# Optimization experiments

Measured on AMD Instinct MI355X. Metric: run time of the kernel, lower is better.

Reference implementation:

```python
import jax, jax.numpy as jnp
import numpy as np

ALPHA = 0.2  # LeakyReLU negative slope
NEG_BIG = -9e15


def setup_inputs() -> dict:
    key = jax.random.key(0)
    k1, k2, k3, k4 = jax.random.split(key, 4)
    N, F_IN, F_OUT = 8192, 256, 64
    h = jax.random.normal(k1, (N, F_IN), dtype=jnp.float32)
    # binary dense adjacency (density ~0.5), kept as float32 as in the torch code
    adj = jax.random.randint(k2, (N, N), 0, 2).astype(jnp.float32)
    W = jax.random.normal(k3, (F_IN, F_OUT), dtype=jnp.float32) * 0.05
    a = jax.random.normal(k4, (2 * F_OUT, 1), dtype=jnp.float32) * 0.05
    return {"h": h, "adj": adj, "W": W, "a": a}


def reference(h, adj, W, a):
    F_OUT = W.shape[1]
    Wh = h @ W                               # [N, F]
    # Decomposed concat-attention score: e_ij = LeakyReLU(a1.Wh_i + a2.Wh_j)
    f_src = Wh @ a[:F_OUT, 0]                # [N]
    f_dst = Wh @ a[F_OUT:, 0]                # [N]
    e = f_src[:, None] + f_dst[None, :]      # [N, N]
    e = jnp.where(e > 0, e, ALPHA * e)       # LeakyReLU
    e = jnp.where(adj > 0, e, NEG_BIG)       # mask non-edges
    attention = jax.nn.softmax(e, axis=1)    # row softmax (dropout p=0 -> identity)
    h_prime = attention @ (adj @ Wh)         # note: double propagation as in source
    # concat=True -> ELU
    return jnp.where(h_prime > 0, h_prime, jnp.expm1(h_prime))
```

## Files before the change

kernel.cpp:

```cpp
#include <hip/hip_runtime.h>
#include <hip/hip_bf16.h>


#define N 8192

typedef float f32x4 __attribute__((ext_vector_type(4)));
typedef short s16x8 __attribute__((ext_vector_type(8)));
typedef unsigned long long u64;
typedef u64 u64x2 __attribute__((ext_vector_type(2)));

__device__ __forceinline__ unsigned short f2bf(float x) {
  unsigned u = __float_as_uint(x);
  u += 0x7FFFu + ((u >> 16) & 1u);
  return (unsigned short)(u >> 16);
}
__device__ __forceinline__ unsigned pack2(unsigned short lo, unsigned short hi) {
  return (unsigned)lo | ((unsigned)hi << 16);
}

#define MFMA __builtin_amdgcn_mfma_f32_16x16x32_bf16

__global__ __launch_bounds__(256) void kA(const float* __restrict__ adj,
                                          const float* __restrict__ h,
                                          const float* __restrict__ W,
                                          const float* __restrict__ a,
                                          u64* __restrict__ ML,
                                          unsigned short* __restrict__ Bpack,
                                          float* __restrict__ f,
                                          float* __restrict__ g,
                                          float* __restrict__ expg,
                                          float* __restrict__ expg2) {
  const int l = threadIdx.x & 63;
  const int w = threadIdx.x >> 6;
  const int i = (blockIdx.x << 1) + (w & 1);
  if (w < 2) {
    const float* ap = adj + (size_t)i * N + (l << 2);
    u64* mp = ML + (size_t)i * 128;
    f32x4 v0 = *(const f32x4*)(ap);
    f32x4 v1 = *(const f32x4*)(ap + 256);
    f32x4 v2 = *(const f32x4*)(ap + 512);
    f32x4 v3 = *(const f32x4*)(ap + 768);
    for (int cc = 0; cc < 32; cc += 4) {
      const int cn = (cc < 28) ? (cc + 4) : cc;
      f32x4 n0 = *(const f32x4*)(ap + ((cn + 0) << 8));
      f32x4 n1 = *(const f32x4*)(ap + ((cn + 1) << 8));
      f32x4 n2 = *(const f32x4*)(ap + ((cn + 2) << 8));
      f32x4 n3 = *(const f32x4*)(ap + ((cn + 3) << 8));
      u64 b0  = __ballot(v0.x > 0.f), b1  = __ballot(v0.y > 0.f);
      u64 b2  = __ballot(v0.z > 0.f), b3  = __ballot(v0.w > 0.f);
      u64 b4  = __ballot(v1.x > 0.f), b5  = __ballot(v1.y > 0.f);
      u64 b6  = __ballot(v1.z > 0.f), b7  = __ballot(v1.w > 0.f);
      u64 b8  = __ballot(v2.x > 0.f), b9  = __ballot(v2.y > 0.f);
      u64 b10 = __ballot(v2.z > 0.f), b11 = __ballot(v2.w > 0.f);
      u64 b12 = __ballot(v3.x > 0.f), b13 = __ballot(v3.y > 0.f);
      u64 b14 = __ballot(v3.z > 0.f), b15 = __ballot(v3.w > 0.f);
      if (l == 0) {
        u64x2* q = (u64x2*)(mp + (cc << 2));
        u64x2 t0; t0.x = b0;  t0.y = b1;  q[0] = t0;
        u64x2 t1; t1.x = b2;  t1.y = b3;  q[1] = t1;
        u64x2 t2; t2.x = b4;  t2.y = b5;  q[2] = t2;
        u64x2 t3; t3.x = b6;  t3.y = b7;  q[3] = t3;
        u64x2 t4; t4.x = b8;  t4.y = b9;  q[4] = t4;
        u64x2 t5; t5.x = b10; t5.y = b11; q[5] = t5;
        u64x2 t6; t6.x = b12; t6.y = b13; q[6] = t6;
        u64x2 t7; t7.x = b14; t7.y = b15; q[7] = t7;
      }
      v0 = n0; v1 = n1; v2 = n2; v3 = n3;
    }
  } else {
    const float* hrow = h + (size_t)i * 256;
    float acc = 0.f;
#pragma unroll 4
    for (int kb = 0; kb < 64; ++kb) {
      f32x4 hv = *(const f32x4*)(hrow + (kb << 2));
      acc += hv.x * W[((kb << 2) + 0) * 64 + l];
      acc += hv.y * W[((kb << 2) + 1) * 64 + l];
      acc += hv.z * W[((kb << 2) + 2) * 64 + l];
      acc += hv.w * W[((kb << 2) + 3) * 64 + l];
    }
    float s1 = acc * a[l];
    float s2 = acc * a[64 + l];
#pragma unroll
    for (int d = 32; d > 0; d >>= 1) {
      s1 += __shfl_xor(s1, d);
      s2 += __shfl_xor(s2, d);
    }
    if (l == 0) {
      f[i] = s1; g[i] = s2;
      expg[i] = __expf(s2);
      expg2[i] = __expf(0.2f * s2);
    }
    const int kb = i >> 5;
    const int b = l >> 4;
    const int lp = (l & 15) | (((i >> 3) & 3) << 4);
    const int e = i & 7;
    Bpack[(((size_t)(kb * 4 + b)) * 64 + lp) * 8 + e] = f2bf(acc);
  }
}

__global__ __launch_bounds__(512) void k2b(const u64* __restrict__ ML,
                                           const unsigned short* __restrict__ Bpack,
                                           const float* __restrict__ g,
                                           const float* __restrict__ f,
                                           unsigned short* __restrict__ Upack,
                                           float* __restrict__ Av,
                                           float* __restrict__ Cv) {
  __shared__ float red[2][8][64][16];
  __shared__ float gred[2][8][16];
  const int l = threadIdx.x & 63;
  const int w = threadIdx.x >> 6;
  const int i0 = blockIdx.x << 5;
  const int r = l & 15, kg = l >> 4;
  const s16x8* Bv = (const s16x8*)Bpack;
  const u64x2* mrow0 = (const u64x2*)(ML + (size_t)(i0 + r) * 128);
  const u64x2* mrow1 = (const u64x2*)(ML + (size_t)(i0 + 16 + r) * 128);
  const int sh0 = kg << 1;
  f32x4 x0 = {0.f,0.f,0.f,0.f}, x1 = x0, x2 = x0, x3 = x0;
  f32x4 y0 = x0, y1 = x0, y2 = x0, y3 = x0;
  float gmx0 = -INFINITY, gmx1 = -INFINITY;
  for (int cc = 0; cc < 4; ++cc) {
    const int c = (w << 2) + cc;
    u64x2 ma = mrow0[(c << 1)], mb = mrow0[(c << 1) + 1];
    const u64 xa0 = ma.x >> sh0, xa1 = ma.y >> sh0,
              xa2 = mb.x >> sh0, xa3 = mb.y >> sh0;
    u64x2 mc = mrow1[(c << 1)], md = mrow1[(c << 1) + 1];
    const u64 ya0 = mc.x >> sh0, ya1 = mc.y >> sh0,
              ya2 = md.x >> sh0, ya3 = md.y >> sh0;
#pragma unroll
    for (int j7 = 0; j7 < 8; ++j7) {
      const int jb = (c << 3) + j7;
      f32x4 g0 = *(const f32x4*)(g + (jb << 5) + (kg << 3));
      f32x4 g1 = *(const f32x4*)(g + (jb << 5) + (kg << 3) + 4);
      const unsigned p0 = (unsigned)(xa0 >> (j7 << 3)) & 1u;
      const unsigned p1 = (unsigned)(xa1 >> (j7 << 3)) & 1u;
      const unsigned p2 = (unsigned)(xa2 >> (j7 << 3)) & 1u;
      const unsigned p3 = (unsigned)(xa3 >> (j7 << 3)) & 1u;
      const unsigned p4 = (unsigned)(xa0 >> ((j7 << 3) + 1)) & 1u;
      const unsigned p5 = (unsigned)(xa1 >> ((j7 << 3) + 1)) & 1u;
      const unsigned p6 = (unsigned)(xa2 >> ((j7 << 3) + 1)) & 1u;
      const unsigned p7 = (unsigned)(xa3 >> ((j7 << 3) + 1)) & 1u;
      const unsigned q0 = (unsigned)(ya0 >> (j7 << 3)) & 1u;
      const unsigned q1 = (unsigned)(ya1 >> (j7 << 3)) & 1u;
      const unsigned q2 = (unsigned)(ya2 >> (j7 << 3)) & 1u;
      const unsigned q3 = (unsigned)(ya3 >> (j7 << 3)) & 1u;
      const unsigned q4 = (unsigned)(ya0 >> ((j7 << 3) + 1)) & 1u;
      const unsigned q5 = (unsigned)(ya1 >> ((j7 << 3) + 1)) & 1u;
      const unsigned q6 = (unsigned)(ya2 >> ((j7 << 3) + 1)) & 1u;
      const unsigned q7 = (unsigned)(ya3 >> ((j7 << 3) + 1)) & 1u;
      s16x8 af0, af1;
      af0[0] = p0 ? (short)0x3F80 : (short)0;
      af0[1] = p1 ? (short)0x3F80 : (short)0;
      af0[2] = p2 ? (short)0x3F80 : (short)0;
      af0[3] = p3 ? (short)0x3F80 : (short)0;
      af0[4] = p4 ? (short)0x3F80 : (short)0;
      af0[5] = p5 ? (short)0x3F80 : (short)0;
      af0[6] = p6 ? (short)0x3F80 : (short)0;
      af0[7] = p7 ? (short)0x3F80 : (short)0;
      af1[0] = q0 ? (short)0x3F80 : (short)0;
      af1[1] = q1 ? (short)0x3F80 : (short)0;
      af1[2] = q2 ? (short)0x3F80 : (short)0;
      af1[3] = q3 ? (short)0x3F80 : (short)0;
      af1[4] = q4 ? (short)0x3F80 : (short)0;
      af1[5] = q5 ? (short)0x3F80 : (short)0;
      af1[6] = q6 ? (short)0x3F80 : (short)0;
      af1[7] = q7 ? (short)0x3F80 : (short)0;
      if (p0) gmx0 = fmaxf(gmx0, g0.x);
      if (p1) gmx0 = fmaxf(gmx0, g0.y);
      if (p2) gmx0 = fmaxf(gmx0, g0.z);
      if (p3) gmx0 = fmaxf(gmx0, g0.w);
      if (p4) gmx0 = fmaxf(gmx0, g1.x);
      if (p5) gmx0 = fmaxf(gmx0, g1.y);
      if (p6) gmx0 = fmaxf(gmx0, g1.z);
      if (p7) gmx0 = fmaxf(gmx0, g1.w);
      if (q0) gmx1 = fmaxf(gmx1, g0.x);
      if (q1) gmx1 = fmaxf(gmx1, g0.y);
      if (q2) gmx1 = fmaxf(gmx1, g0.z);
      if (q3) gmx1 = fmaxf(gmx1, g0.w);
      if (q4) gmx1 = fmaxf(gmx1, g1.x);
      if (q5) gmx1 = fmaxf(gmx1, g1.y);
      if (q6) gmx1 = fmaxf(gmx1, g1.z);
      if (q7) gmx1 = fmaxf(gmx1, g1.w);
      const size_t bi = ((size_t)jb << 8) + l;
      s16x8 f0 = Bv[bi], f1 = Bv[bi + 64], f2 = Bv[bi + 128], f3 = Bv[bi + 192];
      x0 = MFMA(af0, f0, x0, 0, 0, 0);
      x1 = MFMA(af0, f1, x1, 0, 0, 0);
      x2 = MFMA(af0, f2, x2, 0, 0, 0);
      x3 = MFMA(af0, f3, x3, 0, 0, 0);
      y0 = MFMA(af1, f0, y0, 0, 0, 0);
      y1 = MFMA(af1, f1, y1, 0, 0, 0);
      y2 = MFMA(af1, f2, y2, 0, 0, 0);
      y3 = MFMA(af1, f3, y3, 0, 0, 0);
    }
  }
  gmx0 = fmaxf(gmx0, __shfl_xor(gmx0, 16));
  gmx0 = fmaxf(gmx0, __shfl_xor(gmx0, 32));
  gmx1 = fmaxf(gmx1, __shfl_xor(gmx1, 16));
  gmx1 = fmaxf(gmx1, __shfl_xor(gmx1, 32));
  if (l < 16) { gred[0][w][l] = gmx0; gred[1][w][l] = gmx1; }
#pragma unroll
  for (int q = 0; q < 4; ++q) {
    red[0][w][l][q] = x0[q]; red[0][w][l][4 + q] = x1[q];
    red[0][w][l][8 + q] = x2[q]; red[0][w][l][12 + q] = x3[q];
    red[1][w][l][q] = y0[q]; red[1][w][l][4 + q] = y1[q];
    red[1][w][l][8 + q] = y2[q]; red[1][w][l][12 + q] = y3[q];
  }
  __syncthreads();
  const int tl = threadIdx.x & 63;
  const int b = (threadIdx.x >> 6) & 3;
  const int sE = threadIdx.x >> 8;
  const int reg0 = sE << 1;
#pragma unroll
  for (int s = 0; s < 2; ++s) {
    float u0 = 0.f, u1 = 0.f;
#pragma unroll
    for (int w8 = 0; w8 < 8; ++w8) {
      u0 += red[s][w8][tl][(b << 2) + reg0];
      u1 += red[s][w8][tl][(b << 2) + reg0 + 1];
    }
    const int k0 = i0 + (s << 4) + ((tl >> 4) << 2) + reg0;
    const unsigned pkv = pack2(f2bf(u0), f2bf(u1));
    const int kbD = k0 >> 5, lgrp = (k0 >> 3) & 3, e0 = k0 & 7;
    *(unsigned*)((char*)Upack +
        ((size_t)((kbD << 2) + b) * 64 + ((tl & 15) | (lgrp << 4))) * 16 + (e0 << 1)) = pkv;
  }
  if (threadIdx.x < 32) {
    const int s2 = threadIdx.x >> 4, rr = threadIdx.x & 15;
    float gm = gred[s2][0][rr];
#pragma unroll
    for (int w8 = 1; w8 < 8; ++w8) gm = fmaxf(gm, gred[s2][w8][rr]);
    const int i = i0 + (s2 << 4) + rr;
    const float fv = f[i];
    float mm = fv + gm;
    mm = fmaxf(mm, 0.2f * mm);
    Av[i] = __expf(fv - mm);
    Cv[i] = __expf(0.2f * fv - mm);
  }
}

__global__ __launch_bounds__(512) void k3(const u64* __restrict__ ML,
                                          const unsigned short* __restrict__ Upack,
                                          const float* __restrict__ f,
                                          const float* __restrict__ expg,
                                          const float* __restrict__ expg2,
                                          const float* __restrict__ Av,
                                          const float* __restrict__ Cv,
                                          float* __restrict__ out) {
  __shared__ float red[2][8][64][16];
  __shared__ float wred[2][8][16];
  const int l = threadIdx.x & 63;
  const int w = threadIdx.x >> 6;
  const int i0 = blockIdx.x << 5;
  const int r = l & 15, kg = l >> 4;
  const float enf0 = __expf(-f[i0 + r]);
  const float enf1 = __expf(-f[i0 + 16 + r]);
  const float Ar0 = Av[i0 + r],      Cr0 = Cv[i0 + r];
  const float Ar1 = Av[i0 + 16 + r], Cr1 = Cv[i0 + 16 + r];
  const s16x8* Uv = (const s16x8*)Upack;
  const u64x2* mrow0 = (const u64x2*)(ML + (size_t)(i0 + r) * 128);
  const u64x2* mrow1 = (const u64x2*)(ML + (size_t)(i0 + 16 + r) * 128);
  const int sh0 = kg << 1;
  f32x4 x0 = {0.f,0.f,0.f,0.f}, x1 = x0, x2 = x0, x3 = x0;
  f32x4 y0 = x0, y1 = x0, y2 = x0, y3 = x0;
  float ws0 = 0.f, ws1 = 0.f;
  for (int cc = 0; cc < 4; ++cc) {
    const int c = (w << 2) + cc;
    u64x2 ma = mrow0[(c << 1)], mb = mrow0[(c << 1) + 1];
    const u64 xa0 = ma.x >> sh0, xa1 = ma.y >> sh0,
              xa2 = mb.x >> sh0, xa3 = mb.y >> sh0;
    u64x2 mc = mrow1[(c << 1)], md = mrow1[(c << 1) + 1];
    const u64 ya0 = mc.x >> sh0, ya1 = mc.y >> sh0,
              ya2 = md.x >> sh0, ya3 = md.y >> sh0;
#pragma unroll
    for (int j7 = 0; j7 < 8; ++j7) {
      const int jb = (c << 3) + j7;
      f32x4 eg0 = *(const f32x4*)(expg + (jb << 5) + (kg << 3));
      f32x4 eg1 = *(const f32x4*)(expg + (jb << 5) + (kg << 3) + 4);
      f32x4 eh0 = *(const f32x4*)(expg2 + (jb << 5) + (kg << 3));
      f32x4 eh1 = *(const f32x4*)(expg2 + (jb << 5) + (kg << 3) + 4);
      s16x8 pf0, pf1;
#define K3W(pf, idx, wq, sh, egv, ehv, enf, Ar, Cr, wsv) {   \
      const unsigned bit_ = (unsigned)((wq) >> (sh)) & 1u;   \
      const bool sg_ = (egv) > (enf);                        \
      float t_ = sg_ ? (Ar) : (Cr);                          \
      float u_ = sg_ ? (egv) : (ehv);                        \
      float wt_ = t_ * u_;                                   \
      wt_ = bit_ ? wt_ : 0.f;                                \
      wsv += wt_; pf[idx] = (short)f2bf(wt_); }
      K3W(pf0, 0, xa0, (j7 << 3),     eg0.x, eh0.x, enf0, Ar0, Cr0, ws0)
      K3W(pf0, 1, xa1, (j7 << 3),     eg0.y, eh0.y, enf0, Ar0, Cr0, ws0)
      K3W(pf0, 2, xa2, (j7 << 3),     eg0.z, eh0.z, enf0, Ar0, Cr0, ws0)
      K3W(pf0, 3, xa3, (j7 << 3),     eg0.w, eh0.w, enf0, Ar0, Cr0, ws0)
      K3W(pf0, 4, xa0, (j7 << 3) + 1, eg1.x, eh1.x, enf0, Ar0, Cr0, ws0)
      K3W(pf0, 5, xa1, (j7 << 3) + 1, eg1.y, eh1.y, enf0, Ar0, Cr0, ws0)
      K3W(pf0, 6, xa2, (j7 << 3) + 1, eg1.z, eh1.z, enf0, Ar0, Cr0, ws0)
      K3W(pf0, 7, xa3, (j7 << 3) + 1, eg1.w, eh1.w, enf0, Ar0, Cr0, ws0)
      K3W(pf1, 0, ya0, (j7 << 3),     eg0.x, eh0.x, enf1, Ar1, Cr1, ws1)
      K3W(pf1, 1, ya1, (j7 << 3),     eg0.y, eh0.y, enf1, Ar1, Cr1, ws1)
      K3W(pf1, 2, ya2, (j7 << 3),     eg0.z, eh0.z, enf1, Ar1, Cr1, ws1)
      K3W(pf1, 3, ya3, (j7 << 3),     eg0.w, eh0.w, enf1, Ar1, Cr1, ws1)
      K3W(pf1, 4, ya0, (j7 << 3) + 1, eg1.x, eh1.x, enf1, Ar1, Cr1, ws1)
      K3W(pf1, 5, ya1, (j7 << 3) + 1, eg1.y, eh1.y, enf1, Ar1, Cr1, ws1)
      K3W(pf1, 6, ya2, (j7 << 3) + 1, eg1.z, eh1.z, enf1, Ar1, Cr1, ws1)
      K3W(pf1, 7, ya3, (j7 << 3) + 1, eg1.w, eh1.w, enf1, Ar1, Cr1, ws1)
#undef K3W
      const size_t bi = ((size_t)jb << 8) + l;
      s16x8 f0 = Uv[bi], f1 = Uv[bi + 64], f2 = Uv[bi + 128], f3 = Uv[bi + 192];
      x0 = MFMA(pf0, f0, x0, 0, 0, 0);
      x1 = MFMA(pf0, f1, x1, 0, 0, 0);
      x2 = MFMA(pf0, f2, x2, 0, 0, 0);
      x3 = MFMA(pf0, f3, x3, 0, 0, 0);
      y0 = MFMA(pf1, f0, y0, 0, 0, 0);
      y1 = MFMA(pf1, f1, y1, 0, 0, 0);
      y2 = MFMA(pf1, f2, y2, 0, 0, 0);
      y3 = MFMA(pf1, f3, y3, 0, 0, 0);
    }
  }
  ws0 += __shfl_xor(ws0, 16);
  ws0 += __shfl_xor(ws0, 32);
  ws1 += __shfl_xor(ws1, 16);
  ws1 += __shfl_xor(ws1, 32);
  if (l < 16) { wred[0][w][l] = ws0; wred[1][w][l] = ws1; }
#pragma unroll
  for (int q = 0; q < 4; ++q) {
    red[0][w][l][q] = x0[q]; red[0][w][l][4 + q] = x1[q];
    red[0][w][l][8 + q] = x2[q]; red[0][w][l][12 + q] = x3[q];
    red[1][w][l][q] = y0[q]; red[1][w][l][4 + q] = y1[q];
    red[1][w][l][8 + q] = y2[q]; red[1][w][l][12 + q] = y3[q];
  }
  __syncthreads();
  const int tl = threadIdx.x & 63;
  const int b = (threadIdx.x >> 6) & 3;
  const int sE = threadIdx.x >> 8;
#pragma unroll
  for (int s = 0; s < 2; ++s) {
#pragma unroll
    for (int q = 0; q < 2; ++q) {
      const int reg = (sE << 1) + q;
      const int idx = (b << 2) + reg;
      const int row = ((tl >> 4) << 2) + reg;
      float sv = 0.f, dv = 0.f;
#pragma unroll
      for (int w8 = 0; w8 < 8; ++w8) {
        sv += red[s][w8][tl][idx];
        dv += wred[s][w8][row];
      }
      dv = (dv > 0.f) ? dv : 1.f;
      float v = sv / dv;
      v = (v > 0.f) ? v : (__expf(v) - 1.f);
      out[(size_t)(i0 + (s << 4) + row) * 64 + (b << 4) + (tl & 15)] = v;
    }
  }
}

extern "C" void kernel_launch(void* const* d_in, const int* in_sizes, int n_in,
                              void* d_out, int out_size, void* d_ws, size_t ws_size,
                              hipStream_t stream) {
  const float* h   = (const float*)d_in[0];
  const float* adj = (const float*)d_in[1];
  const float* W   = (const float*)d_in[2];
  const float* a   = (const float*)d_in[3];
  float* out = (float*)d_out;
  char* ws = (char*)d_ws;
  unsigned short* Bpack = (unsigned short*)(ws);
  unsigned short* Upack = (unsigned short*)(ws + (1u << 20));
  float* f     = (float*)(ws + (2u << 20));
  float* g     = (float*)(ws + (2u << 20) + 1u * 32768u);
  float* expg  = (float*)(ws + (2u << 20) + 2u * 32768u);
  float* expg2 = (float*)(ws + (2u << 20) + 3u * 32768u);
  float* Av    = (float*)(ws + (2u << 20) + 4u * 32768u);
  float* Cv    = (float*)(ws + (2u << 20) + 5u * 32768u);
  u64* ML = (u64*)(ws + (3u << 20));

  hipLaunchKernelGGL(kA,  dim3(4096), dim3(256), 0, stream,
                     adj, h, W, a, ML, Bpack, f, g, expg, expg2);
  hipLaunchKernelGGL(k2b, dim3(256), dim3(512), 0, stream,
                     ML, Bpack, g, f, Upack, Av, Cv);
  hipLaunchKernelGGL(k3,  dim3(256), dim3(512), 0, stream,
                     ML, Upack, f, expg, expg2, Av, Cv, out);
}
```

Before: 138.9 us.

## Drop softmax row-max pass, restructure adjacency bitmask kernel, MFMA row sums

Softmax weights are now built from precomputed exp(f), exp(0.2f) and exp(-f) without subtracting a row maximum, so the max reduction over masked g in k2b goes away. The adjacency-to-bitmask stage now uses dedicated blocks that each process eight strided 256-float chunks with nontemporal loads, separate from the h@W blocks. In k3, row sums of the weights come from an extra MFMA against a ones vector instead of scalar accumulation and shuffles, and bf16 packing uses a cheaper round-half-up. Without max subtraction, exp can overflow for larger scores, so numerical stability depends on the input scale.

```diff
diff --git a/kernel.cpp b/kernel.cpp
--- a/kernel.cpp
+++ b/kernel.cpp
@@ -9,6 +9,8 @@
 typedef unsigned long long u64;
 typedef u64 u64x2 __attribute__((ext_vector_type(2)));
 
+union PF { s16x8 v; unsigned u[4]; };
+
 __device__ __forceinline__ unsigned short f2bf(float x) {
   unsigned u = __float_as_uint(x);
   u += 0x7FFFu + ((u >> 16) & 1u);
@@ -16,6 +18,10 @@
 }
 __device__ __forceinline__ unsigned pack2(unsigned short lo, unsigned short hi) {
   return (unsigned)lo | ((unsigned)hi << 16);
+}
+__device__ __forceinline__ unsigned packrn(float lo, float hi) {
+  return ((__float_as_uint(lo) + 0x8000u) >> 16) |
+         ((__float_as_uint(hi) + 0x8000u) & 0xFFFF0000u);
 }
 
 #define MFMA __builtin_amdgcn_mfma_f32_16x16x32_bf16
@@ -26,48 +32,44 @@
                                           const float* __restrict__ a,
                                           u64* __restrict__ ML,
                                           unsigned short* __restrict__ Bpack,
-                                          float* __restrict__ f,
-                                          float* __restrict__ g,
                                           float* __restrict__ expg,
-                                          float* __restrict__ expg2) {
+                                          float* __restrict__ expg2,
+                                          float* __restrict__ Af,
+                                          float* __restrict__ Cf,
+                                          float* __restrict__ Enf) {
   const int l = threadIdx.x & 63;
   const int w = threadIdx.x >> 6;
-  const int i = (blockIdx.x << 1) + (w & 1);
-  if (w < 2) {
-    const float* ap = adj + (size_t)i * N + (l << 2);
-    u64* mp = ML + (size_t)i * 128;
-    f32x4 v0 = *(const f32x4*)(ap);
-    f32x4 v1 = *(const f32x4*)(ap + 256);
-    f32x4 v2 = *(const f32x4*)(ap + 512);
-    f32x4 v3 = *(const f32x4*)(ap + 768);
-    for (int cc = 0; cc < 32; cc += 4) {
-      const int cn = (cc < 28) ? (cc + 4) : cc;
-      f32x4 n0 = *(const f32x4*)(ap + ((cn + 0) << 8));
-      f32x4 n1 = *(const f32x4*)(ap + ((cn + 1) << 8));
-      f32x4 n2 = *(const f32x4*)(ap + ((cn + 2) << 8));
-      f32x4 n3 = *(const f32x4*)(ap + ((cn + 3) << 8));
-      u64 b0  = __ballot(v0.x > 0.f), b1  = __ballot(v0.y > 0.f);
-      u64 b2  = __ballot(v0.z > 0.f), b3  = __ballot(v0.w > 0.f);
-      u64 b4  = __ballot(v1.x > 0.f), b5  = __ballot(v1.y > 0.f);
-      u64 b6  = __ballot(v1.z > 0.f), b7  = __ballot(v1.w > 0.f);
-      u64 b8  = __ballot(v2.x > 0.f), b9  = __ballot(v2.y > 0.f);
-      u64 b10 = __ballot(v2.z > 0.f), b11 = __ballot(v2.w > 0.f);
-      u64 b12 = __ballot(v3.x > 0.f), b13 = __ballot(v3.y > 0.f);
-      u64 b14 = __ballot(v3.z > 0.f), b15 = __ballot(v3.w > 0.f);
-      if (l == 0) {
-        u64x2* q = (u64x2*)(mp + (cc << 2));
-        u64x2 t0; t0.x = b0;  t0.y = b1;  q[0] = t0;
-        u64x2 t1; t1.x = b2;  t1.y = b3;  q[1] = t1;
-        u64x2 t2; t2.x = b4;  t2.y = b5;  q[2] = t2;
-        u64x2 t3; t3.x = b6;  t3.y = b7;  q[3] = t3;
-        u64x2 t4; t4.x = b8;  t4.y = b9;  q[4] = t4;
-        u64x2 t5; t5.x = b10; t5.y = b11; q[5] = t5;
-        u64x2 t6; t6.x = b12; t6.y = b13; q[6] = t6;
-        u64x2 t7; t7.x = b14; t7.y = b15; q[7] = t7;
-      }
-      v0 = n0; v1 = n1; v2 = n2; v3 = n3;
+  const int bid = blockIdx.x;
+  if (bid < 1024) {
+    const int wid = (bid << 2) + w;
+    for (int it = 0; it < 8; ++it) {
+      const int ch0 = wid + it * 32768;
+      f32x4 v0 = __builtin_nontemporal_load((const f32x4*)(adj + (((size_t)(ch0          )) << 8) + (l << 2)));
+      f32x4 v1 = __builtin_nontemporal_load((const f32x4*)(adj + (((size_t)(ch0 +  4096)) << 8) + (l << 2)));
+      f32x4 v2 = __builtin_nontemporal_load((const f32x4*)(adj + (((size_t)(ch0 +  8192)) << 8) + (l << 2)));
+      f32x4 v3 = __builtin_nontemporal_load((const f32x4*)(adj + (((size_t)(ch0 + 12288)) << 8) + (l << 2)));
+      f32x4 v4 = __builtin_nontemporal_load((const f32x4*)(adj + (((size_t)(ch0 + 16384)) << 8) + (l << 2)));
+      f32x4 v5 = __builtin_nontemporal_load((const f32x4*)(adj + (((size_t)(ch0 + 20480)) << 8) + (l << 2)));
+      f32x4 v6 = __builtin_nontemporal_load((const f32x4*)(adj + (((size_t)(ch0 + 24576)) << 8) + (l << 2)));
+      f32x4 v7 = __builtin_nontemporal_load((const f32x4*)(adj + (((size_t)(ch0 + 28672)) << 8) + (l << 2)));
+#define KCHUNK(vk, koff) {                                                    \
+      const int ch = ch0 + (koff);                                            \
+      u64 b0 = __ballot(vk.x > 0.f);                                          \
+      u64 b1 = __ballot(vk.y > 0.f);                                          \
+      u64 b2 = __ballot(vk.z > 0.f);                                          \
+      u64 b3 = __ballot(vk.w > 0.f);                                          \
+      if (l == 0) {                                                           \
+        u64x2* q = (u64x2*)(ML + (((size_t)(ch >> 5)) << 7) + ((ch & 31) << 2)); \
+        u64x2 t0; t0.x = b0; t0.y = b1;                                       \
+        u64x2 t1; t1.x = b2; t1.y = b3;                                       \
+        q[0] = t0; q[1] = t1;                                                 \
+      } }
+      KCHUNK(v0, 0)     KCHUNK(v1, 4096)  KCHUNK(v2, 8192)  KCHUNK(v3, 12288)
+      KCHUNK(v4, 16384) KCHUNK(v5, 20480) KCHUNK(v6, 24576) KCHUNK(v7, 28672)
+#undef KCHUNK
     }
   } else {
+    const int i = ((bid - 1024) << 2) + w;
     const float* hrow = h + (size_t)i * 256;
     float acc = 0.f;
 #pragma unroll 4
@@ -86,9 +88,11 @@
       s2 += __shfl_xor(s2, d);
     }
     if (l == 0) {
-      f[i] = s1; g[i] = s2;
-      expg[i] = __expf(s2);
+      expg[i]  = __expf(s2);
       expg2[i] = __expf(0.2f * s2);
+      Af[i]    = __expf(s1);
+      Cf[i]    = __expf(0.2f * s1);
+      Enf[i]   = __expf(-s1);
     }
     const int kb = i >> 5;
     const int b = l >> 4;
@@ -100,13 +104,8 @@
 
 __global__ __launch_bounds__(512) void k2b(const u64* __restrict__ ML,
                                            const unsigned short* __restrict__ Bpack,
-                                           const float* __restrict__ g,
-                                           const float* __restrict__ f,
-                                           unsigned short* __restrict__ Upack,
-                                           float* __restrict__ Av,
-                                           float* __restrict__ Cv) {
+                                           unsigned short* __restrict__ Upack) {
   __shared__ float red[2][8][64][16];
-  __shared__ float gred[2][8][16];
   const int l = threadIdx.x & 63;
   const int w = threadIdx.x >> 6;
   const int i0 = blockIdx.x << 5;
@@ -117,7 +116,6 @@
   const int sh0 = kg << 1;
   f32x4 x0 = {0.f,0.f,0.f,0.f}, x1 = x0, x2 = x0, x3 = x0;
   f32x4 y0 = x0, y1 = x0, y2 = x0, y3 = x0;
-  float gmx0 = -INFINITY, gmx1 = -INFINITY;
   for (int cc = 0; cc < 4; ++cc) {
     const int c = (w << 2) + cc;
     u64x2 ma = mrow0[(c << 1)], mb = mrow0[(c << 1) + 1];
@@ -129,8 +127,6 @@
 #pragma unroll
     for (int j7 = 0; j7 < 8; ++j7) {
       const int jb = (c << 3) + j7;
-      f32x4 g0 = *(const f32x4*)(g + (jb << 5) + (kg << 3));
-      f32x4 g1 = *(const f32x4*)(g + (jb << 5) + (kg << 3) + 4);
       const unsigned p0 = (unsigned)(xa0 >> (j7 << 3)) & 1u;
       const unsigned p1 = (unsigned)(xa1 >> (j7 << 3)) & 1u;
       const unsigned p2 = (unsigned)(xa2 >> (j7 << 3)) & 1u;
@@ -164,22 +160,6 @@
       af1[5] = q5 ? (short)0x3F80 : (short)0;
       af1[6] = q6 ? (short)0x3F80 : (short)0;
       af1[7] = q7 ? (short)0x3F80 : (short)0;
-      if (p0) gmx0 = fmaxf(gmx0, g0.x);
-      if (p1) gmx0 = fmaxf(gmx0, g0.y);
-      if (p2) gmx0 = fmaxf(gmx0, g0.z);
-      if (p3) gmx0 = fmaxf(gmx0, g0.w);
-      if (p4) gmx0 = fmaxf(gmx0, g1.x);
-      if (p5) gmx0 = fmaxf(gmx0, g1.y);
-      if (p6) gmx0 = fmaxf(gmx0, g1.z);
-      if (p7) gmx0 = fmaxf(gmx0, g1.w);
-      if (q0) gmx1 = fmaxf(gmx1, g0.x);
-      if (q1) gmx1 = fmaxf(gmx1, g0.y);
-      if (q2) gmx1 = fmaxf(gmx1, g0.z);
-      if (q3) gmx1 = fmaxf(gmx1, g0.w);
-      if (q4) gmx1 = fmaxf(gmx1, g1.x);
-      if (q5) gmx1 = fmaxf(gmx1, g1.y);
-      if (q6) gmx1 = fmaxf(gmx1, g1.z);
-      if (q7) gmx1 = fmaxf(gmx1, g1.w);
       const size_t bi = ((size_t)jb << 8) + l;
       s16x8 f0 = Bv[bi], f1 = Bv[bi + 64], f2 = Bv[bi + 128], f3 = Bv[bi + 192];
       x0 = MFMA(af0, f0, x0, 0, 0, 0);
@@ -192,11 +172,6 @@
       y3 = MFMA(af1, f3, y3, 0, 0, 0);
     }
   }
-  gmx0 = fmaxf(gmx0, __shfl_xor(gmx0, 16));
-  gmx0 = fmaxf(gmx0, __shfl_xor(gmx0, 32));
-  gmx1 = fmaxf(gmx1, __shfl_xor(gmx1, 16));
-  gmx1 = fmaxf(gmx1, __shfl_xor(gmx1, 32));
-  if (l < 16) { gred[0][w][l] = gmx0; gred[1][w][l] = gmx1; }
 #pragma unroll
   for (int q = 0; q < 4; ++q) {
     red[0][w][l][q] = x0[q]; red[0][w][l][4 + q] = x1[q];
@@ -223,27 +198,15 @@
     *(unsigned*)((char*)Upack +
         ((size_t)((kbD << 2) + b) * 64 + ((tl & 15) | (lgrp << 4))) * 16 + (e0 << 1)) = pkv;
   }
-  if (threadIdx.x < 32) {
-    const int s2 = threadIdx.x >> 4, rr = threadIdx.x & 15;
-    float gm = gred[s2][0][rr];
-#pragma unroll
-    for (int w8 = 1; w8 < 8; ++w8) gm = fmaxf(gm, gred[s2][w8][rr]);
-    const int i = i0 + (s2 << 4) + rr;
-    const float fv = f[i];
-    float mm = fv + gm;
-    mm = fmaxf(mm, 0.2f * mm);
-    Av[i] = __expf(fv - mm);
-    Cv[i] = __expf(0.2f * fv - mm);
-  }
 }
 
 __global__ __launch_bounds__(512) void k3(const u64* __restrict__ ML,
                                           const unsigned short* __restrict__ Upack,
-                                          const float* __restrict__ f,
                                           const float* __restrict__ expg,
                                           const float* __restrict__ expg2,
-                                          const float* __restrict__ Av,
-                                          const float* __restrict__ Cv,
+                                          const float* __restrict__ Af,
+                                          const float* __restrict__ Cf,
+                                          const float* __restrict__ Enf,
                                           float* __restrict__ out) {
   __shared__ float red[2][8][64][16];
   __shared__ float wred[2][8][16];
@@ -251,17 +214,17 @@
   const int w = threadIdx.x >> 6;
   const int i0 = blockIdx.x << 5;
   const int r = l & 15, kg = l >> 4;
-  const float enf0 = __expf(-f[i0 + r]);
-  const float enf1 = __expf(-f[i0 + 16 + r]);
-  const float Ar0 = Av[i0 + r],      Cr0 = Cv[i0 + r];
-  const float Ar1 = Av[i0 + 16 + r], Cr1 = Cv[i0 + 16 + r];
+  const float enf0 = Enf[i0 + r],      enf1 = Enf[i0 + 16 + r];
+  const float Ar0 = Af[i0 + r],        Cr0 = Cf[i0 + r];
+  const float Ar1 = Af[i0 + 16 + r],   Cr1 = Cf[i0 + 16 + r];
   const s16x8* Uv = (const s16x8*)Upack;
   const u64x2* mrow0 = (const u64x2*)(ML + (size_t)(i0 + r) * 128);
   const u64x2* mrow1 = (const u64x2*)(ML + (size_t)(i0 + 16 + r) * 128);
   const int sh0 = kg << 1;
-  f32x4 x0 = {0.f,0.f,0.f,0.f}, x1 = x0, x2 = x0, x3 = x0;
-  f32x4 y0 = x0, y1 = x0, y2 = x0, y3 = x0;
-  float ws0 = 0.f, ws1 = 0.f;
+  const s16x8 ones = {(short)0x3F80, (short)0x3F80, (short)0x3F80, (short)0x3F80,
+                      (short)0x3F80, (short)0x3F80, (short)0x3F80, (short)0x3F80};
+  f32x4 x0 = {0.f,0.f,0.f,0.f}, x1 = x0, x2 = x0, x3 = x0, xd = x0;
+  f32x4 y0 = x0, y1 = x0, y2 = x0, y3 = x0, yd = x0;
   for (int cc = 0; cc < 4; ++cc) {
     const int c = (w << 2) + cc;
     u64x2 ma = mrow0[(c << 1)], mb = mrow0[(c << 1) + 1];
@@ -277,49 +240,52 @@
       f32x4 eg1 = *(const f32x4*)(expg + (jb << 5) + (kg << 3) + 4);
       f32x4 eh0 = *(const f32x4*)(expg2 + (jb << 5) + (kg << 3));
       f32x4 eh1 = *(const f32x4*)(expg2 + (jb << 5) + (kg << 3) + 4);
-      s16x8 pf0, pf1;
-#define K3W(pf, idx, wq, sh, egv, ehv, enf, Ar, Cr, wsv) {   \
-      const unsigned bit_ = (unsigned)((wq) >> (sh)) & 1u;   \
-      const bool sg_ = (egv) > (enf);                        \
-      float t_ = sg_ ? (Ar) : (Cr);                          \
-      float u_ = sg_ ? (egv) : (ehv);                        \
-      float wt_ = t_ * u_;                                   \
-      wt_ = bit_ ? wt_ : 0.f;                                \
-      wsv += wt_; pf[idx] = (short)f2bf(wt_); }
-      K3W(pf0, 0, xa0, (j7 << 3),     eg0.x, eh0.x, enf0, Ar0, Cr0, ws0)
-      K3W(pf0, 1, xa1, (j7 << 3),     eg0.y, eh0.y, enf0, Ar0, Cr0, ws0)
-      K3W(pf0, 2, xa2, (j7 << 3),     eg0.z, eh0.z, enf0, Ar0, Cr0, ws0)
-      K3W(pf0, 3, xa3, (j7 << 3),     eg0.w, eh0.w, enf0, Ar0, Cr0, ws0)
-      K3W(pf0, 4, xa0, (j7 << 3) + 1, eg1.x, eh1.x, enf0, Ar0, Cr0, ws0)
-      K3W(pf0, 5, xa1, (j7 << 3) + 1, eg1.y, eh1.y, enf0, Ar0, Cr0, ws0)
-      K3W(pf0, 6, xa2, (j7 << 3) + 1, eg1.z, eh1.z, enf0, Ar0, Cr0, ws0)
-      K3W(pf0, 7, xa3, (j7 << 3) + 1, eg1.w, eh1.w, enf0, Ar0, Cr0, ws0)
-      K3W(pf1, 0, ya0, (j7 << 3),     eg0.x, eh0.x, enf1, Ar1, Cr1, ws1)
-      K3W(pf1, 1, ya1, (j7 << 3),     eg0.y, eh0.y, enf1, Ar1, Cr1, ws1)
-      K3W(pf1, 2, ya2, (j7 << 3),     eg0.z, eh0.z, enf1, Ar1, Cr1, ws1)
-      K3W(pf1, 3, ya3, (j7 << 3),     eg0.w, eh0.w, enf1, Ar1, Cr1, ws1)
-      K3W(pf1, 4, ya0, (j7 << 3) + 1, eg1.x, eh1.x, enf1, Ar1, Cr1, ws1)
-      K3W(pf1, 5, ya1, (j7 << 3) + 1, eg1.y, eh1.y, enf1, Ar1, Cr1, ws1)
-      K3W(pf1, 6, ya2, (j7 << 3) + 1, eg1.z, eh1.z, enf1, Ar1, Cr1, ws1)
-      K3W(pf1, 7, ya3, (j7 << 3) + 1, eg1.w, eh1.w, enf1, Ar1, Cr1, ws1)
-#undef K3W
+#define WT(wq, sh, egv, ehv, enf, Ar, Cr)                                    \
+      ((((wq) >> (sh)) & 1ull) ?                                             \
+        (((egv) > (enf)) ? (Ar) * (egv) : (Cr) * (ehv)) : 0.f)
+      const float w00 = WT(xa0, (j7 << 3),     eg0.x, eh0.x, enf0, Ar0, Cr0);
+      const float w01 = WT(xa1, (j7 << 3),     eg0.y, eh0.y, enf0, Ar0, Cr0);
+      const float w02 = WT(xa2, (j7 << 3),     eg0.z, eh0.z, enf0, Ar0, Cr0);
+      const float w03 = WT(xa3, (j7 << 3),     eg0.w, eh0.w, enf0, Ar0, Cr0);
+      const float w04 = WT(xa0, (j7 << 3) + 1, eg1.x, eh1.x, enf0, Ar0, Cr0);
+      const float w05 = WT(xa1, (j7 << 3) + 1, eg1.y, eh1.y, enf0, Ar0, Cr0);
+      const float w06 = WT(xa2, (j7 << 3) + 1, eg1.z, eh1.z, enf0, Ar0, Cr0);
+      const float w07 = WT(xa3, (j7 << 3) + 1, eg1.w, eh1.w, enf0, Ar0, Cr0);
+      const float w10 = WT(ya0, (j7 << 3),     eg0.x, eh0.x, enf1, Ar1, Cr1);
+      const float w11 = WT(ya1, (j7 << 3),     eg0.y, eh0.y, enf1, Ar1, Cr1);
+      const float w12 = WT(ya2, (j7 << 3),     eg0.z, eh0.z, enf1, Ar1, Cr1);
+      const float w13 = WT(ya3, (j7 << 3),     eg0.w, eh0.w, enf1, Ar1, Cr1);
+      const float w14 = WT(ya0, (j7 << 3) + 1, eg1.x, eh1.x, enf1, Ar1, Cr1);
+      const float w15 = WT(ya1, (j7 << 3) + 1, eg1.y, eh1.y, enf1, Ar1, Cr1);
+      const float w16 = WT(ya2, (j7 << 3) + 1, eg1.z, eh1.z, enf1, Ar1, Cr1);
+      const float w17 = WT(ya3, (j7 << 3) + 1, eg1.w, eh1.w, enf1, Ar1, Cr1);
+#undef WT
+      PF pf0, pf1;
+      pf0.u[0] = packrn(w00, w01); pf0.u[1] = packrn(w02, w03);
+      pf0.u[2] = packrn(w04, w05); pf0.u[3] = packrn(w06, w07);
+      pf1.u[0] = packrn(w10, w11); pf1.u[1] = packrn(w12, w13);
+      pf1.u[2] = packrn(w14, w15); pf1.u[3] = packrn(w16, w17);
       const size_t bi = ((size_t)jb << 8) + l;
       s16x8 f0 = Uv[bi], f1 = Uv[bi + 64], f2 = Uv[bi + 128], f3 = Uv[bi + 192];
-      x0 = MFMA(pf0, f0, x0, 0, 0, 0);
-      x1 = MFMA(pf0, f1, x1, 0, 0, 0);
-      x2 = MFMA(pf0, f2, x2, 0, 0, 0);
-      x3 = MFMA(pf0, f3, x3, 0, 0, 0);
-      y0 = MFMA(pf1, f0, y0, 0, 0, 0);
-      y1 = MFMA(pf1, f1, y1, 0, 0, 0);
-      y2 = MFMA(pf1, f2, y2, 0, 0, 0);
-      y3 = MFMA(pf1, f3, y3, 0, 0, 0);
-    }
-  }
-  ws0 += __shfl_xor(ws0, 16);
-  ws0 += __shfl_xor(ws0, 32);
-  ws1 += __shfl_xor(ws1, 16);
-  ws1 += __shfl_xor(ws1, 32);
-  if (l < 16) { wred[0][w][l] = ws0; wred[1][w][l] = ws1; }
+      x0 = MFMA(pf0.v, f0, x0, 0, 0, 0);
+      x1 = MFMA(pf0.v, f1, x1, 0, 0, 0);
+      x2 = MFMA(pf0.v, f2, x2, 0, 0, 0);
+      x3 = MFMA(pf0.v, f3, x3, 0, 0, 0);
+      xd = MFMA(pf0.v, ones, xd, 0, 0, 0);
+      y0 = MFMA(pf1.v, f0, y0, 0, 0, 0);
+      y1 = MFMA(pf1.v, f1, y1, 0, 0, 0);
+      y2 = MFMA(pf1.v, f2, y2, 0, 0, 0);
+      y3 = MFMA(pf1.v, f3, y3, 0, 0, 0);
+      yd = MFMA(pf1.v, ones, yd, 0, 0, 0);
+    }
+  }
+  if (r == 0) {
+#pragma unroll
+    for (int q = 0; q < 4; ++q) {
+      wred[0][w][(kg << 2) + q] = xd[q];
+      wred[1][w][(kg << 2) + q] = yd[q];
+    }
+  }
 #pragma unroll
   for (int q = 0; q < 4; ++q) {
     red[0][w][l][q] = x0[q]; red[0][w][l][4 + q] = x1[q];
@@ -363,18 +329,17 @@
   char* ws = (char*)d_ws;
   unsigned short* Bpack = (unsigned short*)(ws);
   unsigned short* Upack = (unsigned short*)(ws + (1u << 20));
-  float* f     = (float*)(ws + (2u << 20));
-  float* g     = (float*)(ws + (2u << 20) + 1u * 32768u);
-  float* expg  = (float*)(ws + (2u << 20) + 2u * 32768u);
-  float* expg2 = (float*)(ws + (2u << 20) + 3u * 32768u);
-  float* Av    = (float*)(ws + (2u << 20) + 4u * 32768u);
-  float* Cv    = (float*)(ws + (2u << 20) + 5u * 32768u);
+  float* expg  = (float*)(ws + (2u << 20));
+  float* expg2 = (float*)(ws + (2u << 20) + 1u * 32768u);
+  float* Af    = (float*)(ws + (2u << 20) + 2u * 32768u);
+  float* Cf    = (float*)(ws + (2u << 20) + 3u * 32768u);
+  float* Enf   = (float*)(ws + (2u << 20) + 4u * 32768u);
   u64* ML = (u64*)(ws + (3u << 20));
 
-  hipLaunchKernelGGL(kA,  dim3(4096), dim3(256), 0, stream,
-                     adj, h, W, a, ML, Bpack, f, g, expg, expg2);
+  hipLaunchKernelGGL(kA,  dim3(3072), dim3(256), 0, stream,
+                     adj, h, W, a, ML, Bpack, expg, expg2, Af, Cf, Enf);
   hipLaunchKernelGGL(k2b, dim3(256), dim3(512), 0, stream,
-                     ML, Bpack, g, f, Upack, Av, Cv);
+                     ML, Bpack, Upack);
   hipLaunchKernelGGL(k3,  dim3(256), dim3(512), 0, stream,
-                     ML, Upack, f, expg, expg2, Av, Cv, out);
-}
+                     ML, Upack, expg, expg2, Af, Cf, Enf, out);
+}
```

Result: slower. 150.9 us (+8.6%).
